# Kernel optimization log

Hardware: AMD Instinct MI355X
Metric: run time of the kernel (lower is better)

Reference implementation:

```python
import jax, jax.numpy as jnp
import numpy as np
from functools import reduce

IN_CH = 1; OUT_CH = 16; K = 3; PAD = 1; QDEPTH = 2; WIRES = 4; DIM = 2 ** WIRES

# --- precomputed CNOT permutation matrices (constants) ---
# PennyLane convention: wire 0 is the most significant bit of the basis index.
def _cnot_mat(control, target):
    perm = np.arange(DIM)
    cbit = 1 << (WIRES - 1 - control)
    tbit = 1 << (WIRES - 1 - target)
    flip = (perm & cbit).astype(bool)
    perm = np.where(flip, perm ^ tbit, perm)
    return jnp.asarray(np.eye(DIM, dtype=np.complex64)[perm])

# StronglyEntanglingLayers default ranges: r_l = l % (n_wires - 1) + 1
_CNOTS = [[_cnot_mat(i, (i + (l % (WIRES - 1) + 1)) % WIRES) for i in range(WIRES)]
          for l in range(QDEPTH)]

def _rot(angles):
    # qml.Rot(phi, theta, omega) = RZ(omega) @ RY(theta) @ RZ(phi)
    phi, theta, omega = angles[0], angles[1], angles[2]
    c = jnp.cos(theta / 2); s = jnp.sin(theta / 2)
    return jnp.stack([
        jnp.exp(-0.5j * (phi + omega)) * c, -jnp.exp(0.5j * (phi - omega)) * s,
        jnp.exp(-0.5j * (phi - omega)) * s,  jnp.exp(0.5j * (phi + omega)) * c,
    ]).reshape(2, 2)

def _sel_unitary(weights):
    # Full 16x16 unitary of StronglyEntanglingLayers(weights) -- dim is tiny,
    # so building the dense unitary once and batching patches through it is
    # the efficient form (vs. per-gate contractions over 2.1M state vectors).
    U = jnp.eye(DIM, dtype=jnp.complex64)
    for l in range(QDEPTH):
        layer = reduce(jnp.kron, [_rot(weights[l, i]) for i in range(WIRES)])
        U = layer @ U
        for C in _CNOTS[l]:
            U = C @ U
    return U

def setup_inputs() -> dict:
    key = jax.random.key(0)
    k1, k2 = jax.random.split(key)
    x = jax.random.normal(k1, (32, 1, 256, 256), dtype=jnp.float32)
    weights = jax.random.uniform(k2, (QDEPTH, WIRES, 3), dtype=jnp.float32)
    return {"x": x, "weights": weights}

def reference(x, weights):
    b, c, h_in, w_in = x.shape
    h_out = h_in + 2 * PAD - K + 1
    w_out = w_in + 2 * PAD - K + 1
    # ConstantPad2d with value 0.01
    xp = jnp.pad(x, ((0, 0), (0, 0), (PAD, PAD), (PAD, PAD)), constant_values=0.01)
    # unfold -> (b, c*K*K, h_out, w_out), feature order (c, k0, k1)
    patches = jax.lax.conv_general_dilated_patches(xp, (K, K), (1, 1), 'VALID')
    patches = patches.transpose(0, 2, 3, 1).reshape(b * h_out * w_out, K * K)
    # zero-pad patch vectors from K*K=9 to 2^wires=16, then L2-normalize (eps=1e-12)
    patches = jnp.pad(patches, ((0, 0), (0, DIM - K * K)))
    norm = jnp.linalg.norm(patches, axis=-1, keepdims=True)
    patches = patches / jnp.maximum(norm, 1e-12)
    # Mottonen prep on |0> yields the normalized patch exactly (up to global
    # phase); then apply the entangling-layer unitary and measure probs.
    state = patches.astype(jnp.complex64) @ _sel_unitary(weights).T  # (N, 16)
    probs = jnp.abs(state) ** 2
    out = jnp.clip(probs * (DIM * 0.5), 0.0, 1.0)[:, :OUT_CH]
    return out.reshape(b, h_out, w_out, OUT_CH).transpose(0, 3, 1, 2)
```

## Files before the change

kernel.cpp:

```cpp
#include <hip/hip_runtime.h>
#include <math.h>


#define WIRES 4
#define DIM 16

__device__ inline void rot_entry(float phi, float th, float om, int rb, int cb,
                                 float& er, float& ei) {
    float a = 0.5f * (phi + om);
    float b = 0.5f * (phi - om);
    float cc = cosf(0.5f * th), ss = sinf(0.5f * th);
    if (rb == 0 && cb == 0) { er = cc * cosf(a); ei = -cc * sinf(a); }
    else if (rb == 0 && cb == 1) { er = -ss * cosf(b); ei = -ss * sinf(b); }
    else if (rb == 1 && cb == 0) { er = ss * cosf(b); ei = -ss * sinf(b); }
    else { er = cc * cosf(a); ei = cc * sinf(a); }
}

__device__ inline void layer_elem(const float* __restrict__ w, int l, int r,
                                  int c, float& pr, float& pi) {
    pr = 1.f; pi = 0.f;
    #pragma unroll
    for (int i = 0; i < WIRES; ++i) {
        const float* wi = w + (l * WIRES + i) * 3;
        float er, ei;
        int rb = (r >> (3 - i)) & 1, cb = (c >> (3 - i)) & 1;
        rot_entry(wi[0], wi[1], wi[2], rb, cb, er, ei);
        float nr = pr * er - pi * ei;
        float ni = pr * ei + pi * er;
        pr = nr; pi = ni;
    }
}

__device__ inline int cnot_src(int r, int range) {
    int src = r;
    #pragma unroll
    for (int i = WIRES - 1; i >= 0; --i) {
        int control = i, target = (i + range) & 3;
        int cbit = 1 << (3 - control), tbit = 1 << (3 - target);
        if (src & cbit) src ^= tbit;
    }
    return src;
}

__global__ __launch_bounds__(256) void build_unitary(
        const float* __restrict__ w, float* __restrict__ uout) {
    __shared__ float Lr[DIM][DIM], Li[DIM][DIM];
    __shared__ float Ur[DIM][DIM], Ui[DIM][DIM];
    __shared__ float Tr[DIM][DIM], Ti[DIM][DIM];
    int t = threadIdx.x;
    int r = t >> 4, c = t & 15;

    float lr, li;
    layer_elem(w, 0, r, c, lr, li);
    Lr[r][c] = lr; Li[r][c] = li;
    __syncthreads();
    int s0 = cnot_src(r, 1);
    Ur[r][c] = Lr[s0][c]; Ui[r][c] = Li[s0][c];
    __syncthreads();

    layer_elem(w, 1, r, c, lr, li);
    Lr[r][c] = lr; Li[r][c] = li;
    __syncthreads();
    float ar = 0.f, ai = 0.f;
    #pragma unroll
    for (int m = 0; m < DIM; ++m) {
        float xr = Lr[r][m], xi = Li[r][m];
        float yr = Ur[m][c], yi = Ui[m][c];
        ar += xr * yr - xi * yi;
        ai += xr * yi + xi * yr;
    }
    Tr[r][c] = ar; Ti[r][c] = ai;
    __syncthreads();
    int s1 = cnot_src(r, 2);
    uout[r * DIM + c]           = Tr[s1][c];
    uout[256 + r * DIM + c]     = Ti[s1][c];
}

#define H 256
#define W 256
#define NB 32
#define OUTC 16

__global__ __launch_bounds__(256) void qconv_kernel(
        const float* __restrict__ x, const float* __restrict__ u,
        float* __restrict__ out) {
    __shared__ float sUr[OUTC][9];
    __shared__ float sUi[OUTC][9];
    __shared__ float rows[3][W + 8];

    int t = threadIdx.x;
    int blk = blockIdx.x;
    int i = blk & (H - 1);
    int b = blk >> 8;

    if (t < OUTC * 9) {
        int k = t / 9, m = t % 9;
        sUr[k][m] = u[k * DIM + m];
        sUi[k][m] = u[256 + k * DIM + m];
    }

    const float* xb = x + (size_t)b * H * W;
    #pragma unroll
    for (int di = 0; di < 3; ++di) {
        int row = i + di - 1;
        for (int cpos = t; cpos < W + 2; cpos += 256) {
            int j = cpos - 1;
            float v = 0.01f;
            if ((unsigned)row < (unsigned)H && (unsigned)j < (unsigned)W)
                v = xb[row * W + j];
            rows[di][cpos] = v;
        }
    }
    __syncthreads();

    float p[9];
    #pragma unroll
    for (int di = 0; di < 3; ++di)
        #pragma unroll
        for (int dj = 0; dj < 3; ++dj)
            p[di * 3 + dj] = rows[di][t + dj];

    float n2 = 0.f;
    #pragma unroll
    for (int m = 0; m < 9; ++m) n2 = fmaf(p[m], p[m], n2);
    float factor = 8.0f / fmaxf(n2, 1e-24f);

    float* ob = out + (size_t)b * OUTC * H * W + (size_t)i * W + t;
    #pragma unroll
    for (int k = 0; k < OUTC; ++k) {
        float sr = 0.f, si = 0.f;
        #pragma unroll
        for (int m = 0; m < 9; ++m) {
            sr = fmaf(sUr[k][m], p[m], sr);
            si = fmaf(sUi[k][m], p[m], si);
        }
        float v = factor * (sr * sr + si * si);
        ob[(size_t)k * H * W] = fminf(v, 1.0f);
    }
}

extern "C" void kernel_launch(void* const* d_in, const int* in_sizes, int n_in,
                              void* d_out, int out_size, void* d_ws, size_t ws_size,
                              hipStream_t stream) {
    const float* x = (const float*)d_in[0];
    const float* w = (const float*)d_in[1];
    float* out = (float*)d_out;
    float* uws = (float*)d_ws;

    build_unitary<<<1, 256, 0, stream>>>(w, uws);
    qconv_kernel<<<NB * H, 256, 0, stream>>>(x, uws, out);
}
```

Baseline: 173.1 us.

## Process four rows per block with four-pixel register tiles and float4 stores

Each block now covers four output rows and stages six input rows in LDS, which cuts the redundant halo reloads of the old one-row-per-block scheme. Each thread computes four adjacent output pixels from a 3x6 register window, so each coefficient is read from LDS once per four pixels, and results are written as float4. Output stays write-bandwidth bound (32x16x256x256 floats), so most of any gain comes from wider stores and fewer blocks. Register pressure goes up.

```diff
diff --git a/kernel.cpp b/kernel.cpp
--- a/kernel.cpp
+++ b/kernel.cpp
@@ -72,26 +72,28 @@
     Tr[r][c] = ar; Ti[r][c] = ai;
     __syncthreads();
     int s1 = cnot_src(r, 2);
-    uout[r * DIM + c]           = Tr[s1][c];
-    uout[256 + r * DIM + c]     = Ti[s1][c];
+    uout[r * DIM + c]       = Tr[s1][c];
+    uout[256 + r * DIM + c] = Ti[s1][c];
 }
 
 #define H 256
 #define W 256
 #define NB 32
 #define OUTC 16
+#define RPB 4
+#define LDSW 264
 
 __global__ __launch_bounds__(256) void qconv_kernel(
         const float* __restrict__ x, const float* __restrict__ u,
         float* __restrict__ out) {
     __shared__ float sUr[OUTC][9];
     __shared__ float sUi[OUTC][9];
-    __shared__ float rows[3][W + 8];
+    __shared__ float rows[RPB + 2][LDSW];
 
     int t = threadIdx.x;
     int blk = blockIdx.x;
-    int i = blk & (H - 1);
-    int b = blk >> 8;
+    int b  = blk >> 6;
+    int i0 = (blk & 63) * RPB;
 
     if (t < OUTC * 9) {
         int k = t / 9, m = t % 9;
@@ -101,41 +103,69 @@
 
     const float* xb = x + (size_t)b * H * W;
     #pragma unroll
-    for (int di = 0; di < 3; ++di) {
-        int row = i + di - 1;
-        for (int cpos = t; cpos < W + 2; cpos += 256) {
-            int j = cpos - 1;
+    for (int r = 0; r < RPB + 2; ++r) {
+        int gr = i0 + r - 1;
+        for (int c = t; c < W + 2; c += 256) {
+            int j = c - 1;
             float v = 0.01f;
-            if ((unsigned)row < (unsigned)H && (unsigned)j < (unsigned)W)
-                v = xb[row * W + j];
-            rows[di][cpos] = v;
+            if ((unsigned)gr < (unsigned)H && (unsigned)j < (unsigned)W)
+                v = xb[gr * W + j];
+            rows[r][c] = v;
         }
     }
     __syncthreads();
 
-    float p[9];
+    int lr = t >> 6;
+    int j0 = (t & 63) * 4;
+
+    float win[3][6];
     #pragma unroll
-    for (int di = 0; di < 3; ++di)
+    for (int di = 0; di < 3; ++di) {
+        float4 a  = *(const float4*)&rows[lr + di][j0];
+        float2 bb = *(const float2*)&rows[lr + di][j0 + 4];
+        win[di][0] = a.x;  win[di][1] = a.y;  win[di][2] = a.z;
+        win[di][3] = a.w;  win[di][4] = bb.x; win[di][5] = bb.y;
+    }
+
+    float factor[4];
+    #pragma unroll
+    for (int q = 0; q < 4; ++q) {
+        float n2 = 0.f;
         #pragma unroll
-        for (int dj = 0; dj < 3; ++dj)
-            p[di * 3 + dj] = rows[di][t + dj];
+        for (int di = 0; di < 3; ++di)
+            #pragma unroll
+            for (int dj = 0; dj < 3; ++dj) {
+                float v = win[di][q + dj];
+                n2 = fmaf(v, v, n2);
+            }
+        factor[q] = 8.0f / fmaxf(n2, 1e-24f);
+    }
 
-    float n2 = 0.f;
-    #pragma unroll
-    for (int m = 0; m < 9; ++m) n2 = fmaf(p[m], p[m], n2);
-    float factor = 8.0f / fmaxf(n2, 1e-24f);
+    int i = i0 + lr;
+    float* ob = out + ((size_t)b * OUTC * H + i) * W + j0;
 
-    float* ob = out + (size_t)b * OUTC * H * W + (size_t)i * W + t;
-    #pragma unroll
+    #pragma unroll 4
     for (int k = 0; k < OUTC; ++k) {
-        float sr = 0.f, si = 0.f;
+        float cr[9], ci[9];
         #pragma unroll
-        for (int m = 0; m < 9; ++m) {
-            sr = fmaf(sUr[k][m], p[m], sr);
-            si = fmaf(sUi[k][m], p[m], si);
+        for (int m = 0; m < 9; ++m) { cr[m] = sUr[k][m]; ci[m] = sUi[k][m]; }
+        float4 o;
+        float* op = &o.x;
+        #pragma unroll
+        for (int q = 0; q < 4; ++q) {
+            float sr = 0.f, si = 0.f;
+            #pragma unroll
+            for (int di = 0; di < 3; ++di)
+                #pragma unroll
+                for (int dj = 0; dj < 3; ++dj) {
+                    float v = win[di][q + dj];
+                    int m = di * 3 + dj;
+                    sr = fmaf(cr[m], v, sr);
+                    si = fmaf(ci[m], v, si);
+                }
+            op[q] = fminf(factor[q] * (sr * sr + si * si), 1.0f);
         }
-        float v = factor * (sr * sr + si * si);
-        ob[(size_t)k * H * W] = fminf(v, 1.0f);
+        *(float4*)(ob + (size_t)k * H * W) = o;
     }
 }
 
@@ -148,5 +178,5 @@
     float* uws = (float*)d_ws;
 
     build_unitary<<<1, 256, 0, stream>>>(w, uws);
-    qconv_kernel<<<NB * H, 256, 0, stream>>>(x, uws, out);
+    qconv_kernel<<<NB * (H / RPB), 256, 0, stream>>>(x, uws, out);
 }
```

After: 179.0 us. 3.4% more time.
